# Kernel optimization log

Measured on AMD Instinct MI355X. Metric: run time of the kernel, lower is better.

The kernel has to match this reference:

```python
import jax, jax.numpy as jnp
import numpy as np

BLOCKSIZE = 128
KEEPER = 128


def setup_inputs() -> dict:
    key = jax.random.key(0)
    ks = jax.random.split(key, 8)
    S, H = 2048, 4096
    n_nonout = H - KEEPER          # 3968
    nb = n_nonout // BLOCKSIZE     # 31 low-precision blocks
    return {
        "x": jax.random.normal(ks[0], (1, S, H), dtype=jnp.float32),
        "weight": jax.random.normal(ks[1], (H, H), dtype=jnp.float32),   # [out, in]
        "scales": jax.random.uniform(ks[2], (H, n_nonout), dtype=jnp.float32),
        "keep_scales": jax.random.uniform(ks[3], (H, 1), dtype=jnp.float32),
        "inp_scales_lo": jax.random.uniform(ks[4], (S, nb), dtype=jnp.float32),
        "inp_scales_hi": jax.random.uniform(ks[5], (S, 1), dtype=jnp.float32),
        "inp_base_lo": jax.random.uniform(ks[6], (S, nb), dtype=jnp.float32),
        "inp_base_hi": jax.random.uniform(ks[7], (S, 1), dtype=jnp.float32),
    }


def reference(x, weight, scales, keep_scales, inp_scales_lo, inp_scales_hi,
              inp_base_lo, inp_base_hi):
    # Faithful vectorization of QLinearLayer._forward (channel_group == 0, bias None).
    bs, S, H = x.shape
    xs = x[0]                      # [S, H]  (bs == 1 assert in original)
    W = weight.T                   # [H, O]
    n_nonout = H - KEEPER
    nb = n_nonout // BLOCKSIZE
    O = W.shape[1]

    # Per-block weight scales: scales[:, i1] for each block start i1 -> [nb, O]
    w_blk_scales = scales[:, 0:n_nonout:BLOCKSIZE].T              # [nb, O]

    # Blockwise outer-product scaling fused into the operands:
    # y[s,o] = sum_n sc_lo[s,n] * ws[n,o] * (x_block_n @ W_block_n)[s,o]
    x_lo = xs[:, :n_nonout].reshape(S, nb, BLOCKSIZE) * inp_scales_lo[:, :, None]
    W_lo = W[:n_nonout, :].reshape(nb, BLOCKSIZE, O) * w_blk_scales[:, None, :]
    y = x_lo.reshape(S, n_nonout) @ W_lo.reshape(n_nonout, O)     # [S, O]

    # int8 keeper channels (high-precision path)
    hi_scales = inp_scales_hi @ keep_scales.T                      # [S, O]
    y_hi = xs[:, n_nonout:] @ W[n_nonout:, :]                      # [S, O]
    y = y + y_hi * hi_scales

    return y.reshape(bs, S, O)
```

## Files before the change

kernel.cpp:

```cpp
#include <hip/hip_runtime.h>

#define S_DIM 2048
#define K_DIM 4096
#define O_DIM 4096
#define NNON  3968
#define NB    31

#define XBLK 8192
#define WBLK 16384

typedef __bf16 bf16x8 __attribute__((ext_vector_type(8)));
typedef float  f32x4  __attribute__((ext_vector_type(4)));

__device__ __forceinline__ unsigned short f2bf(float f) {
    union { float f; unsigned u; } v; v.f = f;
    unsigned r = v.u + 0x7FFFu + ((v.u >> 16) & 1u);
    return (unsigned short)(r >> 16);
}

__global__ __launch_bounds__(256) void prepass(const float* __restrict__ x,
                                               const float* __restrict__ sc_lo,
                                               const float* __restrict__ sc_hi,
                                               const float* __restrict__ w,
                                               const float* __restrict__ scales,
                                               const float* __restrict__ keep,
                                               unsigned short* __restrict__ A,
                                               unsigned short* __restrict__ B)
{
    const int b = blockIdx.x;
    if (b < XBLK) {
        int idx = b * 256 + threadIdx.x;
        int s = idx >> 10;
        int k = (idx & 1023) << 2;
        float4 v = ((const float4*)x)[idx];
        float sc = (k < NNON) ? sc_lo[s * NB + (k >> 7)] : sc_hi[s];
        ushort4 o;
        o.x = f2bf(v.x * sc); o.y = f2bf(v.y * sc);
        o.z = f2bf(v.z * sc); o.w = f2bf(v.w * sc);
        ((ushort4*)A)[idx] = o;
    } else {
        int idx = (b - XBLK) * 256 + threadIdx.x;
        int o = idx >> 10;
        int k = (idx & 1023) << 2;
        float4 v = ((const float4*)w)[idx];
        float sc = (k < NNON) ? scales[(size_t)o * NNON + ((k >> 7) << 7)] : keep[o];
        ushort4 r;
        r.x = f2bf(v.x * sc); r.y = f2bf(v.y * sc);
        r.z = f2bf(v.z * sc); r.w = f2bf(v.w * sc);
        ((ushort4*)B)[idx] = r;
    }
}

#define BM 128
#define BN 128
#define BK 64

__global__ __launch_bounds__(256) void gemm_bt(const unsigned short* __restrict__ A,
                                               const unsigned short* __restrict__ B,
                                               float* __restrict__ C)
{
    __shared__ unsigned short As[BM * BK];
    __shared__ unsigned short Bs[BN * BK];

    const int tid  = threadIdx.x;
    const int wave = tid >> 6;
    const int lane = tid & 63;
    const int quad = lane >> 4;
    const int l16  = lane & 15;
    const int bm = blockIdx.y * BM;
    const int bn = blockIdx.x * BN;
    const int wm = (wave >> 1) * 64;
    const int wn = (wave & 1) * 64;

    const int srow = (lane >> 3);
    const int scol = (((lane & 7) ^ (srow & 7)) << 3);
    const int swz  = (l16 & 7);

    const unsigned short* Abase = A + (size_t)(bm + wave * 32 + srow) * K_DIM + scol;
    const unsigned short* Bbase = B + (size_t)(bn + wave * 32 + srow) * K_DIM + scol;

    f32x4 acc[4][4];
    #pragma unroll
    for (int i = 0; i < 4; ++i)
        #pragma unroll
        for (int j = 0; j < 4; ++j)
            acc[i][j] = (f32x4){0.f, 0.f, 0.f, 0.f};

    #pragma unroll
    for (int c = 0; c < 4; ++c) {
        __builtin_amdgcn_global_load_lds(
            (__attribute__((address_space(1))) unsigned int*)(Abase + (size_t)(c * 8) * K_DIM),
            (__attribute__((address_space(3))) unsigned int*)(&As[(wave * 4 + c) * 512]),
            16, 0, 0);
        __builtin_amdgcn_global_load_lds(
            (__attribute__((address_space(1))) unsigned int*)(Bbase + (size_t)(c * 8) * K_DIM),
            (__attribute__((address_space(3))) unsigned int*)(&Bs[(wave * 4 + c) * 512]),
            16, 0, 0);
    }
    __syncthreads();

    for (int k0 = 0; k0 < K_DIM; k0 += BK) {
        bf16x8 af[2][4], bfr[2][4];
        #pragma unroll
        for (int ks = 0; ks < 2; ++ks) {
            #pragma unroll
            for (int i = 0; i < 4; ++i)
                af[ks][i] = *(const bf16x8*)(&As[(wm + i * 16 + l16) * BK + (((ks * 4 + quad) ^ swz) << 3)]);
            #pragma unroll
            for (int j = 0; j < 4; ++j)
                bfr[ks][j] = *(const bf16x8*)(&Bs[(wn + j * 16 + l16) * BK + (((ks * 4 + quad) ^ swz) << 3)]);
        }
        __syncthreads();

        if (k0 + BK < K_DIM) {
            const size_t koff = (size_t)(k0 + BK);
            #pragma unroll
            for (int c = 0; c < 4; ++c) {
                __builtin_amdgcn_global_load_lds(
                    (__attribute__((address_space(1))) unsigned int*)(Abase + (size_t)(c * 8) * K_DIM + koff),
                    (__attribute__((address_space(3))) unsigned int*)(&As[(wave * 4 + c) * 512]),
                    16, 0, 0);
                __builtin_amdgcn_global_load_lds(
                    (__attribute__((address_space(1))) unsigned int*)(Bbase + (size_t)(c * 8) * K_DIM + koff),
                    (__attribute__((address_space(3))) unsigned int*)(&Bs[(wave * 4 + c) * 512]),
                    16, 0, 0);
            }
        }

        #pragma unroll
        for (int ks = 0; ks < 2; ++ks)
            #pragma unroll
            for (int i = 0; i < 4; ++i)
                #pragma unroll
                for (int j = 0; j < 4; ++j)
                    acc[i][j] = __builtin_amdgcn_mfma_f32_16x16x32_bf16(af[ks][i], bfr[ks][j], acc[i][j], 0, 0, 0);

        __syncthreads();
    }

    #pragma unroll
    for (int i = 0; i < 4; ++i)
        #pragma unroll
        for (int j = 0; j < 4; ++j) {
            const int col = bn + wn + j * 16 + l16;
            #pragma unroll
            for (int r = 0; r < 4; ++r) {
                const int row = bm + wm + i * 16 + quad * 4 + r;
                C[(size_t)row * O_DIM + col] = acc[i][j][r];
            }
        }
}

extern "C" void kernel_launch(void* const* d_in, const int* in_sizes, int n_in,
                              void* d_out, int out_size, void* d_ws, size_t ws_size,
                              hipStream_t stream) {
    const float* x      = (const float*)d_in[0];
    const float* weight = (const float*)d_in[1];
    const float* scales = (const float*)d_in[2];
    const float* keep   = (const float*)d_in[3];
    const float* sc_lo  = (const float*)d_in[4];
    const float* sc_hi  = (const float*)d_in[5];

    unsigned short* A = (unsigned short*)d_ws;
    unsigned short* B = A + (size_t)S_DIM * K_DIM;

    prepass<<<XBLK + WBLK, 256, 0, stream>>>(x, sc_lo, sc_hi, weight, scales, keep, A, B);

    dim3 grid(O_DIM / BN, S_DIM / BM);
    gemm_bt<<<grid, 256, 0, stream>>>(A, B, (float*)d_out);
}
```

Baseline: 246.8 us.

## Load A fragments directly from global into registers with prefetch, skip LDS

The A operand no longer goes through shared memory. Each wave loads its own A fragments straight from global memory into registers and prefetches the next K-step's fragments while the MFMAs run, so only B is staged through LDS. This removes A's LDS writes and reads and halves the shared-memory footprint. In exchange, A tiles are reloaded redundantly by the two waves that share the same rows, global access becomes less coalesced (16-byte strided row reads), and the extra prefetch registers raise register pressure.

```diff
diff --git a/kernel.cpp b/kernel.cpp
--- a/kernel.cpp
+++ b/kernel.cpp
@@ -59,7 +59,6 @@
                                                const unsigned short* __restrict__ B,
                                                float* __restrict__ C)
 {
-    __shared__ unsigned short As[BM * BK];
     __shared__ unsigned short Bs[BN * BK];
 
     const int tid  = threadIdx.x;
@@ -76,8 +75,11 @@
     const int scol = (((lane & 7) ^ (srow & 7)) << 3);
     const int swz  = (l16 & 7);
 
-    const unsigned short* Abase = A + (size_t)(bm + wave * 32 + srow) * K_DIM + scol;
     const unsigned short* Bbase = B + (size_t)(bn + wave * 32 + srow) * K_DIM + scol;
+    const unsigned short* Arow[4];
+    #pragma unroll
+    for (int i = 0; i < 4; ++i)
+        Arow[i] = A + (size_t)(bm + wm + i * 16 + l16) * K_DIM + quad * 8;
 
     f32x4 acc[4][4];
     #pragma unroll
@@ -87,45 +89,40 @@
             acc[i][j] = (f32x4){0.f, 0.f, 0.f, 0.f};
 
     #pragma unroll
-    for (int c = 0; c < 4; ++c) {
-        __builtin_amdgcn_global_load_lds(
-            (__attribute__((address_space(1))) unsigned int*)(Abase + (size_t)(c * 8) * K_DIM),
-            (__attribute__((address_space(3))) unsigned int*)(&As[(wave * 4 + c) * 512]),
-            16, 0, 0);
+    for (int c = 0; c < 4; ++c)
         __builtin_amdgcn_global_load_lds(
             (__attribute__((address_space(1))) unsigned int*)(Bbase + (size_t)(c * 8) * K_DIM),
             (__attribute__((address_space(3))) unsigned int*)(&Bs[(wave * 4 + c) * 512]),
             16, 0, 0);
-    }
+    bf16x8 af[2][4], afn[2][4];
+    #pragma unroll
+    for (int ks = 0; ks < 2; ++ks)
+        #pragma unroll
+        for (int i = 0; i < 4; ++i)
+            af[ks][i] = *(const bf16x8*)(Arow[i] + ks * 32);
     __syncthreads();
 
     for (int k0 = 0; k0 < K_DIM; k0 += BK) {
-        bf16x8 af[2][4], bfr[2][4];
+        bf16x8 bfr[2][4];
         #pragma unroll
-        for (int ks = 0; ks < 2; ++ks) {
-            #pragma unroll
-            for (int i = 0; i < 4; ++i)
-                af[ks][i] = *(const bf16x8*)(&As[(wm + i * 16 + l16) * BK + (((ks * 4 + quad) ^ swz) << 3)]);
+        for (int ks = 0; ks < 2; ++ks)
             #pragma unroll
             for (int j = 0; j < 4; ++j)
                 bfr[ks][j] = *(const bf16x8*)(&Bs[(wn + j * 16 + l16) * BK + (((ks * 4 + quad) ^ swz) << 3)]);
-        }
         __syncthreads();
 
-        if (k0 + BK < K_DIM) {
-            const size_t koff = (size_t)(k0 + BK);
+        const size_t knxt = (k0 + BK < K_DIM) ? (size_t)(k0 + BK) : (size_t)k0;
+        #pragma unroll
+        for (int c = 0; c < 4; ++c)
+            __builtin_amdgcn_global_load_lds(
+                (__attribute__((address_space(1))) unsigned int*)(Bbase + (size_t)(c * 8) * K_DIM + knxt),
+                (__attribute__((address_space(3))) unsigned int*)(&Bs[(wave * 4 + c) * 512]),
+                16, 0, 0);
+        #pragma unroll
+        for (int ks = 0; ks < 2; ++ks)
             #pragma unroll
-            for (int c = 0; c < 4; ++c) {
-                __builtin_amdgcn_global_load_lds(
-                    (__attribute__((address_space(1))) unsigned int*)(Abase + (size_t)(c * 8) * K_DIM + koff),
-                    (__attribute__((address_space(3))) unsigned int*)(&As[(wave * 4 + c) * 512]),
-                    16, 0, 0);
-                __builtin_amdgcn_global_load_lds(
-                    (__attribute__((address_space(1))) unsigned int*)(Bbase + (size_t)(c * 8) * K_DIM + koff),
-                    (__attribute__((address_space(3))) unsigned int*)(&Bs[(wave * 4 + c) * 512]),
-                    16, 0, 0);
-            }
-        }
+            for (int i = 0; i < 4; ++i)
+                afn[ks][i] = *(const bf16x8*)(Arow[i] + knxt + ks * 32);
 
         #pragma unroll
         for (int ks = 0; ks < 2; ++ks)
@@ -134,6 +131,12 @@
                 #pragma unroll
                 for (int j = 0; j < 4; ++j)
                     acc[i][j] = __builtin_amdgcn_mfma_f32_16x16x32_bf16(af[ks][i], bfr[ks][j], acc[i][j], 0, 0, 0);
+
+        #pragma unroll
+        for (int ks = 0; ks < 2; ++ks)
+            #pragma unroll
+            for (int i = 0; i < 4; ++i)
+                af[ks][i] = afn[ks][i];
 
         __syncthreads();
     }
```

Measured after the change: 322.5 us. 30.7% more time.
